# Kernel tuning notes

Hardware: AMD Instinct MI355X
Metric: run time of the kernel (lower is better)

Reference implementation:

```python
import jax, jax.numpy as jnp
import numpy as np

KNN = 4
H = 0.03


def setup_inputs() -> dict:
    key = jax.random.key(0)
    pc = jax.random.normal(key, (8, 4096, 3), dtype=jnp.float32)  # [B, N, 3]
    return {"pc": pc}


def reference(pc) -> jnp.ndarray:
    sq = jnp.sum(pc * pc, axis=-1)  # [B, N]
    # dist[b, i, j] = || pc[b,i] - pc[b,j] ||^2
    dist = sq[:, :, None] + sq[:, None, :] - 2.0 * jnp.einsum("bid,bjd->bij", pc, pc)
    dist = jnp.maximum(dist, 0.0)
    # k nearest neighbors with offset=1 (skip self): take smallest KNN+1, drop the first
    neg_top, _ = jax.lax.top_k(-dist, KNN + 1)  # sorted descending -> distances ascending
    knn_dist = -neg_top[..., 1:]  # [B, N, KNN]
    weight = jnp.exp(-knn_dist / (H * H))
    loss = jnp.sum(-knn_dist * weight)
    return loss
```

## Files before the change

### kernel.cpp

```cpp
#include <hip/hip_runtime.h>
#include <math.h>

#define NPTS   4096
#define NB     8
#define TILE   64
#define NWAVES 4
#define JCHUNK (NPTS / NWAVES)
#define INV_H2 (1.0f / (0.03f * 0.03f))

__device__ __forceinline__ float med3f(float a, float b, float c) {
#if defined(__has_builtin)
#if __has_builtin(__builtin_amdgcn_fmed3f)
  return __builtin_amdgcn_fmed3f(a, b, c);
#else
  return fminf(c, fmaxf(a, b));
#endif
#else
  return fminf(c, fmaxf(a, b));
#endif
}

template <bool CHECK>
__device__ __forceinline__ void scan_range(const float2* __restrict__ sxy,
                                           const float* __restrict__ sz,
                                           int lo, int hi, int self,
                                           float xi, float yi, float zi,
                                           float& t0, float& t1, float& t2, float& t3) {
#pragma unroll 8
  for (int j = lo; j < hi; ++j) {
    float2 xy = sxy[j];
    float zz  = sz[j];
    float dx = xy.x - xi;
    float dy = xy.y - yi;
    float dz = zz   - zi;
    float d = fmaf(dx, dx, fmaf(dy, dy, dz * dz));
    if (CHECK) d = (j == self) ? 3.0e38f : d;
    t3 = med3f(t2, d, t3);
    t2 = med3f(t1, d, t2);
    t1 = med3f(t0, d, t1);
    t0 = fminf(t0, d);
  }
}

__device__ __forceinline__ void merge4(float a0, float a1, float a2, float a3,
                                       float b0, float b1, float b2, float b3,
                                       float& o0, float& o1, float& o2, float& o3) {
  float L0 = fminf(a0, b3), L1 = fminf(a1, b2), L2 = fminf(a2, b1), L3 = fminf(a3, b0);
  float e0 = fminf(L0, L2), e2 = fmaxf(L0, L2);
  float e1 = fminf(L1, L3), e3 = fmaxf(L1, L3);
  o0 = fminf(e0, e1); o1 = fmaxf(e0, e1);
  o2 = fminf(e2, e3); o3 = fmaxf(e2, e3);
}

__global__ __launch_bounds__(256)
void repulsion_kernel(const float* __restrict__ pc, float* __restrict__ out) {
  __shared__ float2 sxy[NPTS];
  __shared__ float  sz[NPTS];
  __shared__ float4 cand4[NWAVES * TILE];

  const int blk  = blockIdx.x;
  const int b    = blk >> 6;
  const int tile = blk & 63;
  const int tid  = threadIdx.x;
  const float* base = pc + (size_t)b * NPTS * 3;

  for (int k = tid; k < NPTS; k += 256) {
    float x = base[3 * k + 0];
    float y = base[3 * k + 1];
    float z = base[3 * k + 2];
    sxy[k] = make_float2(x, y);
    sz[k]  = z;
  }
  __syncthreads();

  const int w    = tid >> 6;
  const int lane = tid & 63;
  const int self = tile * TILE + lane;

  float2 pxy = sxy[self];
  const float xi = pxy.x, yi = pxy.y, zi = sz[self];

  const float INF = 3.0e38f;
  float t0 = INF, t1 = INF, t2 = INF, t3 = INF;

  const int j0 = w * JCHUNK;
  const int selfwave = tile >> 4;
  if (w == selfwave) {
    const int s0 = tile * TILE;
    scan_range<false>(sxy, sz, j0, s0, self, xi, yi, zi, t0, t1, t2, t3);
    scan_range<true >(sxy, sz, s0, s0 + TILE, self, xi, yi, zi, t0, t1, t2, t3);
    scan_range<false>(sxy, sz, s0 + TILE, j0 + JCHUNK, self, xi, yi, zi, t0, t1, t2, t3);
  } else {
    scan_range<false>(sxy, sz, j0, j0 + JCHUNK, self, xi, yi, zi, t0, t1, t2, t3);
  }

  cand4[w * TILE + lane] = make_float4(t0, t1, t2, t3);
  __syncthreads();

  if (tid < 64) {
    float4 A = cand4[0 * TILE + lane];
    float4 B = cand4[1 * TILE + lane];
    float4 C = cand4[2 * TILE + lane];
    float4 D = cand4[3 * TILE + lane];
    float ab0, ab1, ab2, ab3, cd0, cd1, cd2, cd3;
    merge4(A.x, A.y, A.z, A.w, B.x, B.y, B.z, B.w, ab0, ab1, ab2, ab3);
    merge4(C.x, C.y, C.z, C.w, D.x, D.y, D.z, D.w, cd0, cd1, cd2, cd3);
    float m0 = fminf(ab0, cd3);
    float m1 = fminf(ab1, cd2);
    float m2 = fminf(ab2, cd1);
    float m3 = fminf(ab3, cd0);

    float s = 0.0f;
    s -= m0 * expf(-m0 * INV_H2);
    s -= m1 * expf(-m1 * INV_H2);
    s -= m2 * expf(-m2 * INV_H2);
    s -= m3 * expf(-m3 * INV_H2);

    for (int off = 32; off > 0; off >>= 1) s += __shfl_down(s, off);
    if (lane == 0) atomicAdd(out, s);
  }
}

extern "C" void kernel_launch(void* const* d_in, const int* in_sizes, int n_in,
                              void* d_out, int out_size, void* d_ws, size_t ws_size,
                              hipStream_t stream) {
  const float* pc = (const float*)d_in[0];
  float* out = (float*)d_out;
  hipMemsetAsync(out, 0, sizeof(float), stream);
  repulsion_kernel<<<dim3(NB * (NPTS / TILE)), dim3(256), 0, stream>>>(pc, out);
}
```

Measured before the change: 89.53 us.

## Use GEMM-form distances with packed float4 points and 8 waves per block

Points are stored in shared memory as float4 (x,y,z,|p|^2) and distances are computed as |q|^2 - 2p·q + |p|^2 with three FMAs, replacing the subtract-and-square form and the separate xy/z arrays. The block grows to 8 waves, so each wave scans half as many candidates, and the per-wave top-4 lists are merged with a deeper merge tree. Loading pc with float4 vectors also speeds the global-to-shared staging. The per-candidate ALU and LDS instruction count drops and more waves are available to hide latency, at the cost of more shared memory per block. The GEMM form can differ numerically from direct differences, which is closer to the reference's own formula.

```diff
diff --git a/kernel.cpp b/kernel.cpp
--- a/kernel.cpp
+++ b/kernel.cpp
@@ -4,7 +4,8 @@
 #define NPTS   4096
 #define NB     8
 #define TILE   64
-#define NWAVES 4
+#define NWAVES 8
+#define BLK    (NWAVES * 64)
 #define JCHUNK (NPTS / NWAVES)
 #define INV_H2 (1.0f / (0.03f * 0.03f))
 
@@ -21,19 +22,17 @@
 }
 
 template <bool CHECK>
-__device__ __forceinline__ void scan_range(const float2* __restrict__ sxy,
-                                           const float* __restrict__ sz,
+__device__ __forceinline__ void scan_range(const float4* __restrict__ sP,
                                            int lo, int hi, int self,
-                                           float xi, float yi, float zi,
+                                           float mx, float my, float mz, float sqi,
                                            float& t0, float& t1, float& t2, float& t3) {
 #pragma unroll 8
   for (int j = lo; j < hi; ++j) {
-    float2 xy = sxy[j];
-    float zz  = sz[j];
-    float dx = xy.x - xi;
-    float dy = xy.y - yi;
-    float dz = zz   - zi;
-    float d = fmaf(dx, dx, fmaf(dy, dy, dz * dz));
+    float4 q = sP[j];
+    float t = fmaf(mz, q.z, q.w);
+    t = fmaf(my, q.y, t);
+    t = fmaf(mx, q.x, t);
+    float d = t + sqi;
     if (CHECK) d = (j == self) ? 3.0e38f : d;
     t3 = med3f(t2, d, t3);
     t2 = med3f(t1, d, t2);
@@ -52,10 +51,9 @@
   o2 = fminf(e2, e3); o3 = fmaxf(e2, e3);
 }
 
-__global__ __launch_bounds__(256)
+__global__ __launch_bounds__(BLK)
 void repulsion_kernel(const float* __restrict__ pc, float* __restrict__ out) {
-  __shared__ float2 sxy[NPTS];
-  __shared__ float  sz[NPTS];
+  __shared__ float4 sP[NPTS];
   __shared__ float4 cand4[NWAVES * TILE];
 
   const int blk  = blockIdx.x;
@@ -63,13 +61,20 @@
   const int tile = blk & 63;
   const int tid  = threadIdx.x;
   const float* base = pc + (size_t)b * NPTS * 3;
+  const float4* pcv = (const float4*)base;
 
-  for (int k = tid; k < NPTS; k += 256) {
-    float x = base[3 * k + 0];
-    float y = base[3 * k + 1];
-    float z = base[3 * k + 2];
-    sxy[k] = make_float2(x, y);
-    sz[k]  = z;
+  for (int g = tid; g < NPTS / 4; g += BLK) {
+    float4 a = pcv[3 * g + 0];
+    float4 c = pcv[3 * g + 1];
+    float4 e = pcv[3 * g + 2];
+    float x0 = a.x, y0 = a.y, z0 = a.z;
+    float x1 = a.w, y1 = c.x, z1 = c.y;
+    float x2 = c.z, y2 = c.w, z2 = e.x;
+    float x3 = e.y, y3 = e.z, z3 = e.w;
+    sP[4 * g + 0] = make_float4(x0, y0, z0, fmaf(x0, x0, fmaf(y0, y0, z0 * z0)));
+    sP[4 * g + 1] = make_float4(x1, y1, z1, fmaf(x1, x1, fmaf(y1, y1, z1 * z1)));
+    sP[4 * g + 2] = make_float4(x2, y2, z2, fmaf(x2, x2, fmaf(y2, y2, z2 * z2)));
+    sP[4 * g + 3] = make_float4(x3, y3, z3, fmaf(x3, x3, fmaf(y3, y3, z3 * z3)));
   }
   __syncthreads();
 
@@ -77,21 +82,22 @@
   const int lane = tid & 63;
   const int self = tile * TILE + lane;
 
-  float2 pxy = sxy[self];
-  const float xi = pxy.x, yi = pxy.y, zi = sz[self];
+  float4 me = sP[self];
+  const float mx = -2.0f * me.x, my = -2.0f * me.y, mz = -2.0f * me.z;
+  const float sqi = me.w;
 
   const float INF = 3.0e38f;
   float t0 = INF, t1 = INF, t2 = INF, t3 = INF;
 
   const int j0 = w * JCHUNK;
-  const int selfwave = tile >> 4;
+  const int selfwave = tile >> 3;
   if (w == selfwave) {
     const int s0 = tile * TILE;
-    scan_range<false>(sxy, sz, j0, s0, self, xi, yi, zi, t0, t1, t2, t3);
-    scan_range<true >(sxy, sz, s0, s0 + TILE, self, xi, yi, zi, t0, t1, t2, t3);
-    scan_range<false>(sxy, sz, s0 + TILE, j0 + JCHUNK, self, xi, yi, zi, t0, t1, t2, t3);
+    scan_range<false>(sP, j0, s0, self, mx, my, mz, sqi, t0, t1, t2, t3);
+    scan_range<true >(sP, s0, s0 + TILE, self, mx, my, mz, sqi, t0, t1, t2, t3);
+    scan_range<false>(sP, s0 + TILE, j0 + JCHUNK, self, mx, my, mz, sqi, t0, t1, t2, t3);
   } else {
-    scan_range<false>(sxy, sz, j0, j0 + JCHUNK, self, xi, yi, zi, t0, t1, t2, t3);
+    scan_range<false>(sP, j0, j0 + JCHUNK, self, mx, my, mz, sqi, t0, t1, t2, t3);
   }
 
   cand4[w * TILE + lane] = make_float4(t0, t1, t2, t3);
@@ -102,13 +108,23 @@
     float4 B = cand4[1 * TILE + lane];
     float4 C = cand4[2 * TILE + lane];
     float4 D = cand4[3 * TILE + lane];
+    float4 E = cand4[4 * TILE + lane];
+    float4 F = cand4[5 * TILE + lane];
+    float4 G = cand4[6 * TILE + lane];
+    float4 H4 = cand4[7 * TILE + lane];
     float ab0, ab1, ab2, ab3, cd0, cd1, cd2, cd3;
+    float ef0, ef1, ef2, ef3, gh0, gh1, gh2, gh3;
     merge4(A.x, A.y, A.z, A.w, B.x, B.y, B.z, B.w, ab0, ab1, ab2, ab3);
     merge4(C.x, C.y, C.z, C.w, D.x, D.y, D.z, D.w, cd0, cd1, cd2, cd3);
-    float m0 = fminf(ab0, cd3);
-    float m1 = fminf(ab1, cd2);
-    float m2 = fminf(ab2, cd1);
-    float m3 = fminf(ab3, cd0);
+    merge4(E.x, E.y, E.z, E.w, F.x, F.y, F.z, F.w, ef0, ef1, ef2, ef3);
+    merge4(G.x, G.y, G.z, G.w, H4.x, H4.y, H4.z, H4.w, gh0, gh1, gh2, gh3);
+    float u0, u1, u2, u3, v0, v1, v2, v3;
+    merge4(ab0, ab1, ab2, ab3, cd0, cd1, cd2, cd3, u0, u1, u2, u3);
+    merge4(ef0, ef1, ef2, ef3, gh0, gh1, gh2, gh3, v0, v1, v2, v3);
+    float m0 = fminf(u0, v3);
+    float m1 = fminf(u1, v2);
+    float m2 = fminf(u2, v1);
+    float m3 = fminf(u3, v0);
 
     float s = 0.0f;
     s -= m0 * expf(-m0 * INV_H2);
@@ -127,5 +143,5 @@
   const float* pc = (const float*)d_in[0];
   float* out = (float*)d_out;
   hipMemsetAsync(out, 0, sizeof(float), stream);
-  repulsion_kernel<<<dim3(NB * (NPTS / TILE)), dim3(256), 0, stream>>>(pc, out);
+  repulsion_kernel<<<dim3(NB * (NPTS / TILE)), dim3(BLK), 0, stream>>>(pc, out);
 }
```

Measured after the change: 82.17 us. 1.09x faster.
